# Optimization experiments

Hardware: AMD Instinct MI355X
Metric: run time of the kernel (lower is better)

## Reference

```python
import jax, jax.numpy as jnp
import numpy as np


def haar_level(x):
    """One 2D Haar (periodization-equivalent for even sizes) DWT on [B,K,C,H,W].
    Returns [B,4K,C,H/2,W/2] with per-parent band order (LL, Hx, Hy, Hxy),
    matching the tree's append order yl, yh0, yh1, yh2."""
    B, K, C, H, W = x.shape
    x = x.reshape(B, K, C, H // 2, 2, W // 2, 2)
    a = x[:, :, :, :, 0, :, 0]
    b = x[:, :, :, :, 0, :, 1]
    c = x[:, :, :, :, 1, :, 0]
    d = x[:, :, :, :, 1, :, 1]
    ll = (a + b + c + d) * 0.5
    h1 = (a - b + c - d) * 0.5   # high along width
    h2 = (a + b - c - d) * 0.5   # high along height
    h3 = (a - b - c + d) * 0.5   # diagonal
    out = jnp.stack([ll, h1, h2, h3], axis=2)  # [B,K,4,C,H/2,W/2]
    return out.reshape(B, 4 * K, C, H // 2, W // 2)


def conv2d(x, w, b, stride, pad):
    y = jax.lax.conv_general_dilated(
        x, w, window_strides=(stride, stride),
        padding=[(pad, pad), (pad, pad)],
        dimension_numbers=('NCHW', 'OIHW', 'NCHW'))
    return y + b[None, :, None, None]


def setup_inputs() -> dict:
    key = jax.random.key(0)
    ks = jax.random.split(key, 9)
    s = 0.05
    return {
        'x':        jax.random.normal(ks[0], (64, 3, 224, 224), dtype=jnp.float32),
        'w_s1':     jax.random.normal(ks[1], (192, 3, 7, 7), dtype=jnp.float32) * s,
        'b_s1':     jax.random.normal(ks[2], (192,), dtype=jnp.float32) * s,
        'w_s2':     jax.random.normal(ks[3], (192, 192, 7, 7), dtype=jnp.float32) * s,
        'b_s2':     jax.random.normal(ks[4], (192,), dtype=jnp.float32) * s,
        'w_p':      jax.random.normal(ks[5], (768, 960, 3, 3), dtype=jnp.float32) * s,
        'b_p':      jax.random.normal(ks[6], (768,), dtype=jnp.float32) * s,
        'cls_token': jax.random.normal(ks[7], (1, 1, 768), dtype=jnp.float32),
        'positions': jax.random.normal(ks[8], (50, 768), dtype=jnp.float32),
    }


def reference(x, w_s1, b_s1, w_s2, b_s2, w_p, b_p, cls_token, positions):
    B = x.shape[0]
    # ---- 4-level full Haar wavelet packet tree (vectorized over subbands) ----
    t = x[:, None]                      # [B,1,3,224,224]
    for _ in range(4):
        t = haar_level(t)               # -> [B,256,3,14,14]
    wav = t.reshape(B, 256 * 3, 14, 14)  # [B,768,14,14] (tree concat order)
    # ---- spatial branch: two strided 7x7 convs (224 -> 56 -> 14) ----
    sp = conv2d(x, w_s1, b_s1, stride=4, pad=3)
    sp = conv2d(sp, w_s2, b_s2, stride=4, pad=3)   # [B,192,14,14]
    feat = jnp.concatenate([wav, sp], axis=1)      # [B,960,14,14]
    # ---- patch projection conv 3x3 s2 -> 7x7, flatten to tokens ----
    y = conv2d(feat, w_p, b_p, stride=2, pad=1)    # [B,768,7,7]
    y = y.reshape(B, 768, 49).transpose(0, 2, 1)   # [B,49,768]
    cls = jnp.broadcast_to(cls_token, (B, 1, 768))
    y = jnp.concatenate([cls, y], axis=1) + positions  # [B,50,768]
    return y
```

## Files before the change

### kernel.cpp

```cpp
#include <hip/hip_runtime.h>
#include <stdint.h>

typedef __attribute__((ext_vector_type(8))) short short8;
typedef __attribute__((ext_vector_type(4))) float floatx4;

__device__ inline unsigned short f2bf(float f){
  union { float fv; unsigned int u; } v; v.fv = f;
  unsigned int u = v.u;
  unsigned int r = ((u >> 16) & 1u) + 0x7FFFu;
  return (unsigned short)((u + r) >> 16);
}

__device__ __forceinline__ void async16(const void* g, void* l){
  __builtin_amdgcn_global_load_lds(
      (const __attribute__((address_space(1))) unsigned int*)g,
      (__attribute__((address_space(3))) unsigned int*)l, 16, 0, 0);
}

#define PBAR(N) do {                                              \
    asm volatile("s_waitcnt vmcnt(" #N ")" ::: "memory");          \
    __builtin_amdgcn_s_barrier();                                  \
    asm volatile("" ::: "memory");                                 \
  } while (0)

__global__ void prep_w1(const float* __restrict__ w, unsigned short* __restrict__ w1p){
  int i = blockIdx.x*256 + threadIdx.x;
  if (i >= 192*192) return;
  int k = i % 192, o = i / 192;
  int cc = k >> 3, kx = k & 7;
  unsigned short v = 0;
  if (cc < 21 && kx < 7){
    int c = cc / 7, ky = cc % 7;
    v = f2bf(w[(o*3 + c)*49 + ky*7 + kx]);
  }
  w1p[i] = v;
}
__global__ void prep_w2(const float* __restrict__ w, unsigned short* __restrict__ w2p){
  int i = blockIdx.x*256 + threadIdx.x;
  if (i >= 192*9408) return;
  int k = i % 9408, o = i / 9408;
  int g = k / 192, c = k % 192;
  int ky = g / 7, kx = g % 7;
  w2p[i] = f2bf(w[((o*192 + c)*7 + ky)*7 + kx]);
}
__global__ void prep_w3(const float* __restrict__ w, unsigned short* __restrict__ w3p){
  int i = blockIdx.x*256 + threadIdx.x;
  if (i >= 768*8640) return;
  int k = i % 8640, o = i / 8640;
  int g = k / 960, c = k % 960;
  int ky = g / 3, kx = g % 3;
  w3p[i] = f2bf(w[((o*960 + c)*3 + ky)*3 + kx]);
}
__global__ void prep_zp(unsigned int* __restrict__ zp){
  zp[threadIdx.x] = 0u;
}

__global__ void pad_x2(const float* __restrict__ x, unsigned short* __restrict__ xh2){
  int idx = blockIdx.x*256 + threadIdx.x;
  if (idx >= 64*3*230*56*8) return;
  int kx = idx & 7; int t = idx >> 3;
  int ox = t % 56;  t /= 56;
  int iy = t % 230; t /= 230;
  int row = iy - 3;
  int col = 4*ox - 3 + kx;
  unsigned short v = 0;
  if (row >= 0 && row < 224 && col >= 0 && col < 224)
    v = f2bf(x[((size_t)t*224 + row)*224 + col]);
  xh2[idx] = v;
}

__global__ void wavelet_kernel(const float* __restrict__ x, unsigned short* __restrict__ feat){
  int blk = blockIdx.x;
  int j = blk % 14; blk /= 14;
  int i = blk % 14; blk /= 14;
  int c = blk % 3;  int b = blk / 3;
  int t = threadIdx.x;
  int u = t >> 4, v = t & 15;
  float val = x[((size_t)(b*3 + c)*224 + (i*16 + u))*224 + (j*16 + v)];
  #pragma unroll
  for (int bit = 1; bit < 64; bit <<= 1){
    float p = __shfl_xor(val, bit);
    val = (t & bit) ? (p - val) : (val + p);
  }
  __shared__ float s[256];
  #pragma unroll
  for (int bit = 64; bit < 256; bit <<= 1){
    s[t] = val; __syncthreads();
    float p = s[t ^ bit]; __syncthreads();
    val = (t & bit) ? (p - val) : (val + p);
  }
  s[t] = val; __syncthreads();
  int k = t;
  int d1 = (k>>6)&3, d2 = (k>>4)&3, d3 = (k>>2)&3, d4 = k&3;
  int mr = (d1>>1) | ((d2>>1)<<1) | ((d3>>1)<<2) | ((d4>>1)<<3);
  int mc = (d1&1)  | ((d2&1)<<1)  | ((d3&1)<<2)  | ((d4&1)<<3);
  float outv = s[mr*16 + mc] * 0.0625f;
  feat[((size_t)((b*14 + i)*14 + j))*960 + (k*3 + c)] = f2bf(outv);
}

__global__ __launch_bounds__(256) void conv1_gemm(const unsigned short* __restrict__ xh2,
                                                  const unsigned short* __restrict__ w1p,
                                                  const float* __restrict__ b1,
                                                  unsigned short* __restrict__ sp1){
  __shared__ unsigned short As[2][128*64], Bs[2][64*64];
  int m0 = blockIdx.x*128, n0 = blockIdx.y*64;
  int tid = threadIdx.x, wave = tid >> 6, lane = tid & 63;
  int l16 = lane & 15, quad = lane >> 4;
  int wy = wave >> 1, wx = wave & 1;
  int r8 = lane >> 3, kb = (lane & 7) ^ r8;

  int Abase[4];
  #pragma unroll
  for (int j = 0; j < 4; j++){
    int row = wave*32 + j*8 + r8;
    int m = m0 + row;
    int ox = m % 56; int t = m / 56; int oy = t % 56; int b = t / 56;
    Abase[j] = (b*690 + 4*oy)*448 + ox*8;
  }
  const unsigned short* pB0 = w1p + (n0 + wave*16 + r8)*192 + kb*8;
  const unsigned short* pB1 = pB0 + 8*192;

  int sw = l16 & 7;
  int xo0 = ((quad    ) ^ sw)*8;
  int xo1 = ((quad + 4) ^ sw)*8;
  int aoff[4];
  #pragma unroll
  for (int mt = 0; mt < 4; mt++) aoff[mt] = (wy*64 + mt*16 + l16)*64;
  int boff0 = (wx*32 + l16)*64, boff1 = boff0 + 16*64;

  floatx4 acc[4][2];
  #pragma unroll
  for (int mt = 0; mt < 4; mt++)
    #pragma unroll
    for (int nt = 0; nt < 2; nt++) acc[mt][nt] = (floatx4){0.f,0.f,0.f,0.f};

  auto stage = [&](int i, int buf){
    int cc = i*8 + kb;
    int c = (cc*147) >> 10;
    int ky = cc - 7*c;
    int koff = (c*230 + ky)*448;
    #pragma unroll
    for (int j = 0; j < 4; j++)
      async16(xh2 + Abase[j] + koff, (void*)&As[buf][(wave*32 + j*8)*64]);
    async16(pB0 + i*64, (void*)&Bs[buf][(wave*16    )*64]);
    async16(pB1 + i*64, (void*)&Bs[buf][(wave*16 + 8)*64]);
  };

  stage(0, 0);
  __syncthreads();
  #pragma unroll
  for (int i = 0; i < 3; i++){
    int buf = i & 1;
    if (i < 2) stage(i+1, buf ^ 1);
    #pragma unroll
    for (int ks = 0; ks < 2; ks++){
      int xo = ks ? xo1 : xo0;
      short8 b0 = *(const short8*)&Bs[buf][boff0 + xo];
      short8 b1 = *(const short8*)&Bs[buf][boff1 + xo];
      #pragma unroll
      for (int mt = 0; mt < 4; mt++){
        short8 a = *(const short8*)&As[buf][aoff[mt] + xo];
        acc[mt][0] = __builtin_amdgcn_mfma_f32_16x16x32_bf16(a, b0, acc[mt][0], 0, 0, 0);
        acc[mt][1] = __builtin_amdgcn_mfma_f32_16x16x32_bf16(a, b1, acc[mt][1], 0, 0, 0);
      }
    }
    __syncthreads();
  }

  #pragma unroll
  for (int mt = 0; mt < 4; mt++){
    #pragma unroll
    for (int rg = 0; rg < 4; rg++){
      int row = wy*64 + mt*16 + quad*4 + rg;
      size_t ob = (size_t)(m0 + row)*192;
      #pragma unroll
      for (int nt = 0; nt < 2; nt++){
        int nn = n0 + wx*32 + nt*16 + l16;
        sp1[ob + nn] = f2bf(acc[mt][nt][rg] + b1[nn]);
      }
    }
  }
}

template<int MODE>
__global__ __launch_bounds__(256) void conv_gemm(const unsigned short* __restrict__ Ain,
                                                 const unsigned short* __restrict__ Bt,
                                                 const float* __restrict__ bias,
                                                 const float* __restrict__ pos,
                                                 const unsigned short* __restrict__ zp,
                                                 void* __restrict__ outp){
  constexpr int OH  = (MODE==2) ? 14 : 7;
  constexpr int OW  = OH;
  constexpr int IH  = (MODE==2) ? 56 : 14;
  constexpr int IW  = IH;
  constexpr int Cin = (MODE==2) ? 192 : 960;
  constexpr int KW  = (MODE==2) ? 7 : 3;
  constexpr int S   = (MODE==2) ? 4 : 2;
  constexpr int P   = (MODE==2) ? 3 : 1;
  constexpr int K   = (MODE==2) ? 9408 : 8640;
  constexpr int NIT = K/64;
  constexpr int MTI = (MODE==2) ? 196 : 49;
  constexpr int GRP = (MODE==2) ? 24 : 96;

  int id = blockIdx.x;
  int g = id / GRP, rem = id % GRP;
  int mtile = g*8 + (rem & 7), ntile = rem >> 3;
  if (mtile >= MTI) return;
  int m0 = mtile*64, n0 = ntile*64;

  __shared__ unsigned short As[3][64*64], Bs[3][64*64];
  int tid = threadIdx.x, wave = tid >> 6, lane = tid & 63;
  int l16 = lane & 15, quad = lane >> 4;
  int wy = wave >> 1, wx = wave & 1;

  int r8 = lane >> 3, kb = (lane & 7) ^ r8;
  int rA0 = wave*16 + r8, rA1 = rA0 + 8;

  int m_0 = m0 + rA0;
  int ox0 = m_0 % OW; int t0 = m_0 / OW; int oy0 = t0 % OH; int bb0 = t0 / OH;
  int iyb0 = S*oy0 - P, ixb0 = S*ox0 - P;
  int abase0 = ((bb0*IH + iyb0)*IW + ixb0)*Cin + kb*8;
  int m_1 = m0 + rA1;
  int ox1 = m_1 % OW; int t1 = m_1 / OW; int oy1 = t1 % OH; int bb1 = t1 / OH;
  int iyb1 = S*oy1 - P, ixb1 = S*ox1 - P;
  int abase1 = ((bb1*IH + iyb1)*IW + ixb1)*Cin + kb*8;

  const unsigned short* pB0 = Bt + (size_t)(n0 + rA0)*K + kb*8;
  const unsigned short* pB1 = Bt + (size_t)(n0 + rA1)*K + kb*8;

  int sw = l16 & 7;
  int xo0 = ((quad    ) ^ sw)*8;
  int xo1 = ((quad + 4) ^ sw)*8;
  int aoff0 = (wy*32      + l16)*64;
  int aoff1 = (wy*32 + 16 + l16)*64;
  int boff0 = (wx*32      + l16)*64;
  int boff1 = (wx*32 + 16 + l16)*64;

  floatx4 acc[2][2];
  #pragma unroll
  for (int a = 0; a < 2; a++)
    #pragma unroll
    for (int bq = 0; bq < 2; bq++) acc[a][bq] = (floatx4){0.f,0.f,0.f,0.f};

  int c0 = 0, ky = 0, kx = 0, k0n = 0;

  auto stage = [&](int buf){
    int koff = (ky*IW + kx)*Cin + c0;
    int iy0 = iyb0 + ky, ix0 = ixb0 + kx;
    int iy1 = iyb1 + ky, ix1 = ixb1 + kx;
    const unsigned short* pa0 = ((unsigned)iy0 < (unsigned)IH && (unsigned)ix0 < (unsigned)IW)
                                ? (Ain + (abase0 + koff)) : zp;
    const unsigned short* pa1 = ((unsigned)iy1 < (unsigned)IH && (unsigned)ix1 < (unsigned)IW)
                                ? (Ain + (abase1 + koff)) : zp;
    async16(pa0, (void*)&As[buf][(wave*16    )*64]);
    async16(pa1, (void*)&As[buf][(wave*16 + 8)*64]);
    async16(pB0 + k0n, (void*)&Bs[buf][(wave*16    )*64]);
    async16(pB1 + k0n, (void*)&Bs[buf][(wave*16 + 8)*64]);
    k0n += 64;
    c0 += 64;
    if (c0 == Cin){ c0 = 0; kx++; if (kx == KW){ kx = 0; ky++; } }
  };

  auto compute = [&](int buf){
    #pragma unroll
    for (int ks = 0; ks < 2; ks++){
      int xo = ks ? xo1 : xo0;
      short8 a0 = *(const short8*)&As[buf][aoff0 + xo];
      short8 a1 = *(const short8*)&As[buf][aoff1 + xo];
      short8 b0 = *(const short8*)&Bs[buf][boff0 + xo];
      short8 b1 = *(const short8*)&Bs[buf][boff1 + xo];
      acc[0][0] = __builtin_amdgcn_mfma_f32_16x16x32_bf16(a0, b0, acc[0][0], 0, 0, 0);
      acc[0][1] = __builtin_amdgcn_mfma_f32_16x16x32_bf16(a0, b1, acc[0][1], 0, 0, 0);
      acc[1][0] = __builtin_amdgcn_mfma_f32_16x16x32_bf16(a1, b0, acc[1][0], 0, 0, 0);
      acc[1][1] = __builtin_amdgcn_mfma_f32_16x16x32_bf16(a1, b1, acc[1][1], 0, 0, 0);
    }
  };

  stage(0); stage(1);
  int bc = 0;
  for (int i = 0; i < NIT - 2; i++){
    PBAR(4);
    int bn = bc + 2; if (bn >= 3) bn -= 3;
    stage(bn);
    compute(bc);
    bc = (bc == 2) ? 0 : bc + 1;
  }
  PBAR(4);
  compute(bc);
  bc = (bc == 2) ? 0 : bc + 1;
  PBAR(0);
  compute(bc);

  #pragma unroll
  for (int mt = 0; mt < 2; mt++){
    #pragma unroll
    for (int rg = 0; rg < 4; rg++){
      int row = wy*32 + mt*16 + quad*4 + rg;
      int mm = m0 + row;
      #pragma unroll
      for (int nt = 0; nt < 2; nt++){
        int nn = n0 + wx*32 + nt*16 + l16;
        float v = acc[mt][nt][rg] + bias[nn];
        if (MODE == 2){
          ((unsigned short*)outp)[(size_t)mm*960 + 768 + nn] = f2bf(v);
        } else {
          int b2 = mm / 49;
          int tt = mm - b2*49;
          v += pos[(size_t)(1 + tt)*768 + nn];
          ((float*)outp)[((size_t)(mm + b2 + 1))*768 + nn] = v;
        }
      }
    }
  }
}

__global__ void cls_kernel(const float* __restrict__ cls, const float* __restrict__ pos,
                           float* __restrict__ out){
  int i = blockIdx.x*256 + threadIdx.x;
  if (i >= 64*768) return;
  int e = i % 768, b = i / 768;
  out[(size_t)(b*50)*768 + e] = cls[e] + pos[e];
}

extern "C" void kernel_launch(void* const* d_in, const int* in_sizes, int n_in,
                              void* d_out, int out_size, void* d_ws, size_t ws_size,
                              hipStream_t stream){
  (void)in_sizes; (void)n_in; (void)out_size;
  const float* x    = (const float*)d_in[0];
  const float* w_s1 = (const float*)d_in[1];
  const float* b_s1 = (const float*)d_in[2];
  const float* w_s2 = (const float*)d_in[3];
  const float* b_s2 = (const float*)d_in[4];
  const float* w_p  = (const float*)d_in[5];
  const float* b_p  = (const float*)d_in[6];
  const float* cls  = (const float*)d_in[7];
  const float* pos  = (const float*)d_in[8];
  float* out = (float*)d_out;

  char* ws = (char*)d_ws;
  if (ws_size < 118235136u) return;
  unsigned short* w1p  = (unsigned short*)(ws + 0);
  unsigned short* sp1  = (unsigned short*)(ws + 131072);
  unsigned short* zp   = (unsigned short*)(ws + 77201408u);
  unsigned short* w2p  = (unsigned short*)(ws + 77266944u);
  unsigned short* w3p  = (unsigned short*)(ws + 80879616u);
  unsigned short* feat = (unsigned short*)(ws + 94150656u);
  unsigned short* xh2  = (unsigned short*)(ws + 77266944u);

  prep_w1<<<(192*192 + 255)/256, 256, 0, stream>>>(w_s1, w1p);
  pad_x2<<<(64*3*230*56*8)/256, 256, 0, stream>>>(x, xh2);
  conv1_gemm<<<dim3(1568, 3), 256, 0, stream>>>(xh2, w1p, b_s1, sp1);
  prep_w2<<<(192*9408 + 255)/256, 256, 0, stream>>>(w_s2, w2p);
  prep_w3<<<(768*8640 + 255)/256, 256, 0, stream>>>(w_p, w3p);
  prep_zp<<<1, 64, 0, stream>>>((unsigned int*)zp);
  wavelet_kernel<<<64*3*14*14, 256, 0, stream>>>(x, feat);
  conv_gemm<2><<<600, 256, 0, stream>>>(sp1, w2p, b_s2, nullptr, zp, (void*)feat);
  conv_gemm<3><<<672, 256, 0, stream>>>(feat, w3p, b_p, pos, zp, (void*)out);
  cls_kernel<<<(64*768 + 255)/256, 256, 0, stream>>>(cls, pos, out);
}
```

Measured before the change: 425.6 us.

## Split K across waves in conv GEMM with per-wave pipelines and LDS reduction

```diff
diff --git a/kernel.cpp b/kernel.cpp
--- a/kernel.cpp
+++ b/kernel.cpp
@@ -16,12 +16,6 @@
       (const __attribute__((address_space(1))) unsigned int*)g,
       (__attribute__((address_space(3))) unsigned int*)l, 16, 0, 0);
 }
-
-#define PBAR(N) do {                                              \
-    asm volatile("s_waitcnt vmcnt(" #N ")" ::: "memory");          \
-    __builtin_amdgcn_s_barrier();                                  \
-    asm volatile("" ::: "memory");                                 \
-  } while (0)
 
 __global__ void prep_w1(const float* __restrict__ w, unsigned short* __restrict__ w1p){
   int i = blockIdx.x*256 + threadIdx.x;
@@ -198,7 +192,7 @@
   constexpr int S   = (MODE==2) ? 4 : 2;
   constexpr int P   = (MODE==2) ? 3 : 1;
   constexpr int K   = (MODE==2) ? 9408 : 8640;
-  constexpr int NIT = K/64;
+  constexpr int NSTEP = K/32;
   constexpr int MTI = (MODE==2) ? 196 : 49;
   constexpr int GRP = (MODE==2) ? 24 : 96;
 
@@ -208,108 +202,123 @@
   if (mtile >= MTI) return;
   int m0 = mtile*64, n0 = ntile*64;
 
-  __shared__ unsigned short As[3][64*64], Bs[3][64*64];
+  __shared__ unsigned short smem[32768];
+
   int tid = threadIdx.x, wave = tid >> 6, lane = tid & 63;
   int l16 = lane & 15, quad = lane >> 4;
-  int wy = wave >> 1, wx = wave & 1;
-
-  int r8 = lane >> 3, kb = (lane & 7) ^ r8;
-  int rA0 = wave*16 + r8, rA1 = rA0 + 8;
-
-  int m_0 = m0 + rA0;
-  int ox0 = m_0 % OW; int t0 = m_0 / OW; int oy0 = t0 % OH; int bb0 = t0 / OH;
-  int iyb0 = S*oy0 - P, ixb0 = S*ox0 - P;
-  int abase0 = ((bb0*IH + iyb0)*IW + ixb0)*Cin + kb*8;
-  int m_1 = m0 + rA1;
-  int ox1 = m_1 % OW; int t1 = m_1 / OW; int oy1 = t1 % OH; int bb1 = t1 / OH;
-  int iyb1 = S*oy1 - P, ixb1 = S*ox1 - P;
-  int abase1 = ((bb1*IH + iyb1)*IW + ixb1)*Cin + kb*8;
-
-  const unsigned short* pB0 = Bt + (size_t)(n0 + rA0)*K + kb*8;
-  const unsigned short* pB1 = Bt + (size_t)(n0 + rA1)*K + kb*8;
-
-  int sw = l16 & 7;
-  int xo0 = ((quad    ) ^ sw)*8;
-  int xo1 = ((quad + 4) ^ sw)*8;
-  int aoff0 = (wy*32      + l16)*64;
-  int aoff1 = (wy*32 + 16 + l16)*64;
-  int boff0 = (wx*32      + l16)*64;
-  int boff1 = (wx*32 + 16 + l16)*64;
-
-  floatx4 acc[2][2];
-  #pragma unroll
-  for (int a = 0; a < 2; a++)
-    #pragma unroll
-    for (int bq = 0; bq < 2; bq++) acc[a][bq] = (floatx4){0.f,0.f,0.f,0.f};
-
-  int c0 = 0, ky = 0, kx = 0, k0n = 0;
+
+  unsigned short* wbase = &smem[wave*8192];
+
+  int s0 = (NSTEP*wave) >> 2;
+  int s1 = (NSTEP*(wave+1)) >> 2;
+  int n = s1 - s0;
+
+  int k32 = s0*32;
+  int c0 = k32 % Cin;
+  int gk = k32 / Cin;
+  int kx = gk % KW, ky = gk / KW;
+
+  int rsub = lane >> 2;
+  int soff = ((lane & 3) ^ (rsub & 3)) * 8;
+
+  int Abase[4], iyb[4], ixb[4];
+  const unsigned short* pB[4];
+  #pragma unroll
+  for (int j = 0; j < 4; j++){
+    int R = 16*j + rsub;
+    int m = m0 + R;
+    int ox = m % OW; int t = m / OW; int oy = t % OH; int b = t / OH;
+    iyb[j] = S*oy - P; ixb[j] = S*ox - P;
+    Abase[j] = ((b*IH + iyb[j])*IW + ixb[j])*Cin;
+    pB[j] = Bt + (size_t)(n0 + R)*K + k32 + soff;
+  }
+
+  int fro = l16*32 + ((quad ^ (l16 & 3)) * 8);
+
+  floatx4 acc[4][4];
+  #pragma unroll
+  for (int mi = 0; mi < 4; mi++)
+    #pragma unroll
+    for (int ni = 0; ni < 4; ni++) acc[mi][ni] = (floatx4){0.f,0.f,0.f,0.f};
 
   auto stage = [&](int buf){
     int koff = (ky*IW + kx)*Cin + c0;
-    int iy0 = iyb0 + ky, ix0 = ixb0 + kx;
-    int iy1 = iyb1 + ky, ix1 = ixb1 + kx;
-    const unsigned short* pa0 = ((unsigned)iy0 < (unsigned)IH && (unsigned)ix0 < (unsigned)IW)
-                                ? (Ain + (abase0 + koff)) : zp;
-    const unsigned short* pa1 = ((unsigned)iy1 < (unsigned)IH && (unsigned)ix1 < (unsigned)IW)
-                                ? (Ain + (abase1 + koff)) : zp;
-    async16(pa0, (void*)&As[buf][(wave*16    )*64]);
-    async16(pa1, (void*)&As[buf][(wave*16 + 8)*64]);
-    async16(pB0 + k0n, (void*)&Bs[buf][(wave*16    )*64]);
-    async16(pB1 + k0n, (void*)&Bs[buf][(wave*16 + 8)*64]);
-    k0n += 64;
-    c0 += 64;
+    #pragma unroll
+    for (int j = 0; j < 4; j++){
+      int iy = iyb[j] + ky, ix = ixb[j] + kx;
+      bool v = ((unsigned)iy < (unsigned)IH) & ((unsigned)ix < (unsigned)IW);
+      const unsigned short* src = v ? (Ain + Abase[j] + koff + soff) : (zp + soff);
+      async16(src, (void*)(wbase + buf*2048 + j*512));
+    }
+    #pragma unroll
+    for (int j = 0; j < 4; j++){
+      async16(pB[j], (void*)(wbase + 4096 + buf*2048 + j*512));
+      pB[j] += 32;
+    }
+    c0 += 32;
     if (c0 == Cin){ c0 = 0; kx++; if (kx == KW){ kx = 0; ky++; } }
   };
 
   auto compute = [&](int buf){
-    #pragma unroll
-    for (int ks = 0; ks < 2; ks++){
-      int xo = ks ? xo1 : xo0;
-      short8 a0 = *(const short8*)&As[buf][aoff0 + xo];
-      short8 a1 = *(const short8*)&As[buf][aoff1 + xo];
-      short8 b0 = *(const short8*)&Bs[buf][boff0 + xo];
-      short8 b1 = *(const short8*)&Bs[buf][boff1 + xo];
-      acc[0][0] = __builtin_amdgcn_mfma_f32_16x16x32_bf16(a0, b0, acc[0][0], 0, 0, 0);
-      acc[0][1] = __builtin_amdgcn_mfma_f32_16x16x32_bf16(a0, b1, acc[0][1], 0, 0, 0);
-      acc[1][0] = __builtin_amdgcn_mfma_f32_16x16x32_bf16(a1, b0, acc[1][0], 0, 0, 0);
-      acc[1][1] = __builtin_amdgcn_mfma_f32_16x16x32_bf16(a1, b1, acc[1][1], 0, 0, 0);
-    }
+    const unsigned short* Ab = wbase + buf*2048;
+    const unsigned short* Bb = wbase + 4096 + buf*2048;
+    short8 a[4], b[4];
+    #pragma unroll
+    for (int i = 0; i < 4; i++){
+      a[i] = *(const short8*)&Ab[fro + i*512];
+      b[i] = *(const short8*)&Bb[fro + i*512];
+    }
+    #pragma unroll
+    for (int mi = 0; mi < 4; mi++)
+      #pragma unroll
+      for (int ni = 0; ni < 4; ni++)
+        acc[mi][ni] = __builtin_amdgcn_mfma_f32_16x16x32_bf16(a[mi], b[ni], acc[mi][ni], 0, 0, 0);
   };
 
   stage(0); stage(1);
-  int bc = 0;
-  for (int i = 0; i < NIT - 2; i++){
-    PBAR(4);
-    int bn = bc + 2; if (bn >= 3) bn -= 3;
-    stage(bn);
-    compute(bc);
-    bc = (bc == 2) ? 0 : bc + 1;
-  }
-  PBAR(4);
-  compute(bc);
-  bc = (bc == 2) ? 0 : bc + 1;
-  PBAR(0);
-  compute(bc);
-
-  #pragma unroll
-  for (int mt = 0; mt < 2; mt++){
-    #pragma unroll
-    for (int rg = 0; rg < 4; rg++){
-      int row = wy*32 + mt*16 + quad*4 + rg;
-      int mm = m0 + row;
+  for (int i = 0; i < n-2; i++){
+    asm volatile("s_waitcnt vmcnt(8)" ::: "memory");
+    compute(i & 1);
+    asm volatile("s_waitcnt lgkmcnt(0)" ::: "memory");
+    stage(i & 1);
+  }
+  asm volatile("s_waitcnt vmcnt(8)" ::: "memory");
+  compute(n & 1);
+  asm volatile("s_waitcnt vmcnt(0)" ::: "memory");
+  compute((n-1) & 1);
+
+  asm volatile("s_waitcnt lgkmcnt(0) vmcnt(0)" ::: "memory");
+  __builtin_amdgcn_sched_barrier(0);
+  float* red = (float*)wbase;
+  #pragma unroll
+  for (int mi = 0; mi < 4; mi++)
+    #pragma unroll
+    for (int ni = 0; ni < 4; ni++)
       #pragma unroll
-      for (int nt = 0; nt < 2; nt++){
-        int nn = n0 + wx*32 + nt*16 + l16;
-        float v = acc[mt][nt][rg] + bias[nn];
-        if (MODE == 2){
-          ((unsigned short*)outp)[(size_t)mm*960 + 768 + nn] = f2bf(v);
-        } else {
-          int b2 = mm / 49;
-          int tt = mm - b2*49;
-          v += pos[(size_t)(1 + tt)*768 + nn];
-          ((float*)outp)[((size_t)(mm + b2 + 1))*768 + nn] = v;
-        }
+      for (int rg = 0; rg < 4; rg++){
+        int row = mi*16 + quad*4 + rg;
+        int col = ni*16 + l16;
+        red[row*64 + col] = acc[mi][ni][rg];
       }
+  __syncthreads();
+  const float* r0 = (const float*)&smem[0];
+  const float* r1 = (const float*)&smem[8192];
+  const float* r2 = (const float*)&smem[16384];
+  const float* r3 = (const float*)&smem[24576];
+  #pragma unroll
+  for (int j = 0; j < 16; j++){
+    int e = tid + 256*j;
+    float v = r0[e] + r1[e] + r2[e] + r3[e];
+    int col = e & 63, row = e >> 6;
+    int mm = m0 + row, nn = n0 + col;
+    v += bias[nn];
+    if (MODE == 2){
+      ((unsigned short*)outp)[(size_t)mm*960 + 768 + nn] = f2bf(v);
+    } else {
+      int b2 = mm / 49;
+      int tt = mm - b2*49;
+      v += pos[(size_t)(1 + tt)*768 + nn];
+      ((float*)outp)[((size_t)(mm + b2 + 1))*768 + nn] = v;
     }
   }
 }
```

Result: slower. 484.7 us (+13.9%).

## Split K across wave pairs in conv GEMM with LDS reduction

Applied to the files above, without the earlier changes.

```diff
diff --git a/kernel.cpp b/kernel.cpp
--- a/kernel.cpp
+++ b/kernel.cpp
@@ -211,7 +211,7 @@
   __shared__ unsigned short As[3][64*64], Bs[3][64*64];
   int tid = threadIdx.x, wave = tid >> 6, lane = tid & 63;
   int l16 = lane & 15, quad = lane >> 4;
-  int wy = wave >> 1, wx = wave & 1;
+  int kh = wave >> 1, nh = wave & 1;
 
   int r8 = lane >> 3, kb = (lane & 7) ^ r8;
   int rA0 = wave*16 + r8, rA1 = rA0 + 8;
@@ -229,18 +229,18 @@
   const unsigned short* pB1 = Bt + (size_t)(n0 + rA1)*K + kb*8;
 
   int sw = l16 & 7;
-  int xo0 = ((quad    ) ^ sw)*8;
-  int xo1 = ((quad + 4) ^ sw)*8;
-  int aoff0 = (wy*32      + l16)*64;
-  int aoff1 = (wy*32 + 16 + l16)*64;
-  int boff0 = (wx*32      + l16)*64;
-  int boff1 = (wx*32 + 16 + l16)*64;
-
-  floatx4 acc[2][2];
-  #pragma unroll
-  for (int a = 0; a < 2; a++)
-    #pragma unroll
-    for (int bq = 0; bq < 2; bq++) acc[a][bq] = (floatx4){0.f,0.f,0.f,0.f};
+  int xo = ((kh*4 + quad) ^ sw)*8;
+  int aoff[4];
+  #pragma unroll
+  for (int mt = 0; mt < 4; mt++) aoff[mt] = (mt*16 + l16)*64;
+  int boff0 = (nh*32      + l16)*64;
+  int boff1 = (nh*32 + 16 + l16)*64;
+
+  floatx4 acc[4][2];
+  #pragma unroll
+  for (int mt = 0; mt < 4; mt++)
+    #pragma unroll
+    for (int nt = 0; nt < 2; nt++) acc[mt][nt] = (floatx4){0.f,0.f,0.f,0.f};
 
   int c0 = 0, ky = 0, kx = 0, k0n = 0;
 
@@ -262,18 +262,20 @@
   };
 
   auto compute = [&](int buf){
-    #pragma unroll
-    for (int ks = 0; ks < 2; ks++){
-      int xo = ks ? xo1 : xo0;
-      short8 a0 = *(const short8*)&As[buf][aoff0 + xo];
-      short8 a1 = *(const short8*)&As[buf][aoff1 + xo];
-      short8 b0 = *(const short8*)&Bs[buf][boff0 + xo];
-      short8 b1 = *(const short8*)&Bs[buf][boff1 + xo];
-      acc[0][0] = __builtin_amdgcn_mfma_f32_16x16x32_bf16(a0, b0, acc[0][0], 0, 0, 0);
-      acc[0][1] = __builtin_amdgcn_mfma_f32_16x16x32_bf16(a0, b1, acc[0][1], 0, 0, 0);
-      acc[1][0] = __builtin_amdgcn_mfma_f32_16x16x32_bf16(a1, b0, acc[1][0], 0, 0, 0);
-      acc[1][1] = __builtin_amdgcn_mfma_f32_16x16x32_bf16(a1, b1, acc[1][1], 0, 0, 0);
-    }
+    short8 b0 = *(const short8*)&Bs[buf][boff0 + xo];
+    short8 b1 = *(const short8*)&Bs[buf][boff1 + xo];
+    short8 a0 = *(const short8*)&As[buf][aoff[0] + xo];
+    short8 a1 = *(const short8*)&As[buf][aoff[1] + xo];
+    short8 a2 = *(const short8*)&As[buf][aoff[2] + xo];
+    short8 a3 = *(const short8*)&As[buf][aoff[3] + xo];
+    acc[0][0] = __builtin_amdgcn_mfma_f32_16x16x32_bf16(a0, b0, acc[0][0], 0, 0, 0);
+    acc[0][1] = __builtin_amdgcn_mfma_f32_16x16x32_bf16(a0, b1, acc[0][1], 0, 0, 0);
+    acc[1][0] = __builtin_amdgcn_mfma_f32_16x16x32_bf16(a1, b0, acc[1][0], 0, 0, 0);
+    acc[1][1] = __builtin_amdgcn_mfma_f32_16x16x32_bf16(a1, b1, acc[1][1], 0, 0, 0);
+    acc[2][0] = __builtin_amdgcn_mfma_f32_16x16x32_bf16(a2, b0, acc[2][0], 0, 0, 0);
+    acc[2][1] = __builtin_amdgcn_mfma_f32_16x16x32_bf16(a2, b1, acc[2][1], 0, 0, 0);
+    acc[3][0] = __builtin_amdgcn_mfma_f32_16x16x32_bf16(a3, b0, acc[3][0], 0, 0, 0);
+    acc[3][1] = __builtin_amdgcn_mfma_f32_16x16x32_bf16(a3, b1, acc[3][1], 0, 0, 0);
   };
 
   stage(0); stage(1);
@@ -291,23 +293,39 @@
   PBAR(0);
   compute(bc);
 
-  #pragma unroll
-  for (int mt = 0; mt < 2; mt++){
-    #pragma unroll
-    for (int rg = 0; rg < 4; rg++){
-      int row = wy*32 + mt*16 + quad*4 + rg;
-      int mm = m0 + row;
+  __syncthreads();
+  float* red = (float*)As;
+  if (kh == 1){
+    #pragma unroll
+    for (int mt = 0; mt < 4; mt++)
       #pragma unroll
-      for (int nt = 0; nt < 2; nt++){
-        int nn = n0 + wx*32 + nt*16 + l16;
-        float v = acc[mt][nt][rg] + bias[nn];
-        if (MODE == 2){
-          ((unsigned short*)outp)[(size_t)mm*960 + 768 + nn] = f2bf(v);
-        } else {
-          int b2 = mm / 49;
-          int tt = mm - b2*49;
-          v += pos[(size_t)(1 + tt)*768 + nn];
-          ((float*)outp)[((size_t)(mm + b2 + 1))*768 + nn] = v;
+      for (int nt = 0; nt < 2; nt++)
+        #pragma unroll
+        for (int rg = 0; rg < 4; rg++){
+          int row = mt*16 + quad*4 + rg;
+          red[nh*2112 + row*33 + nt*16 + l16] = acc[mt][nt][rg];
+        }
+  }
+  __syncthreads();
+  if (kh == 0){
+    #pragma unroll
+    for (int mt = 0; mt < 4; mt++){
+      #pragma unroll
+      for (int rg = 0; rg < 4; rg++){
+        int row = mt*16 + quad*4 + rg;
+        int mm = m0 + row;
+        #pragma unroll
+        for (int nt = 0; nt < 2; nt++){
+          int nn = n0 + nh*32 + nt*16 + l16;
+          float v = acc[mt][nt][rg] + red[nh*2112 + row*33 + nt*16 + l16] + bias[nn];
+          if (MODE == 2){
+            ((unsigned short*)outp)[(size_t)mm*960 + 768 + nn] = f2bf(v);
+          } else {
+            int b2 = mm / 49;
+            int tt = mm - b2*49;
+            v += pos[(size_t)(1 + tt)*768 + nn];
+            ((float*)outp)[((size_t)(mm + b2 + 1))*768 + nn] = v;
+          }
         }
       }
     }
```

Result: no change. 432.9 us (+1.7%).

## Split-K conv GEMMs with atomic fp32 partials and separate bias epilogues

Applied to the files above, without the earlier changes.

```diff
diff --git a/kernel.cpp b/kernel.cpp
--- a/kernel.cpp
+++ b/kernel.cpp
@@ -53,6 +53,10 @@
 }
 __global__ void prep_zp(unsigned int* __restrict__ zp){
   zp[threadIdx.x] = 0u;
+}
+__global__ void zero_f32(float* __restrict__ p, int n){
+  int i = blockIdx.x*256 + threadIdx.x;
+  if (i < n) p[i] = 0.f;
 }
 
 __global__ void pad_x2(const float* __restrict__ x, unsigned short* __restrict__ xh2){
@@ -183,12 +187,10 @@
 }
 
 template<int MODE>
-__global__ __launch_bounds__(256) void conv_gemm(const unsigned short* __restrict__ Ain,
-                                                 const unsigned short* __restrict__ Bt,
-                                                 const float* __restrict__ bias,
-                                                 const float* __restrict__ pos,
-                                                 const unsigned short* __restrict__ zp,
-                                                 void* __restrict__ outp){
+__global__ __launch_bounds__(256) void conv_split(const unsigned short* __restrict__ Ain,
+                                                  const unsigned short* __restrict__ Bt,
+                                                  const unsigned short* __restrict__ zp,
+                                                  float* __restrict__ pout){
   constexpr int OH  = (MODE==2) ? 14 : 7;
   constexpr int OW  = OH;
   constexpr int IH  = (MODE==2) ? 56 : 14;
@@ -198,64 +200,64 @@
   constexpr int S   = (MODE==2) ? 4 : 2;
   constexpr int P   = (MODE==2) ? 3 : 1;
   constexpr int K   = (MODE==2) ? 9408 : 8640;
-  constexpr int NIT = K/64;
-  constexpr int MTI = (MODE==2) ? 196 : 49;
-  constexpr int GRP = (MODE==2) ? 24 : 96;
+  constexpr int K3  = K/3;
+  constexpr int NB  = K3/64;
+  constexpr int MTI = (MODE==2) ? 98 : 25;
+  constexpr int NTI = (MODE==2) ? 2 : 8;
+  constexpr int M   = (MODE==2) ? 12544 : 3136;
+  constexpr int NF  = (MODE==2) ? 192 : 768;
 
   int id = blockIdx.x;
-  int g = id / GRP, rem = id % GRP;
-  int mtile = g*8 + (rem & 7), ntile = rem >> 3;
-  if (mtile >= MTI) return;
-  int m0 = mtile*64, n0 = ntile*64;
-
-  __shared__ unsigned short As[3][64*64], Bs[3][64*64];
-  int tid = threadIdx.x, wave = tid >> 6, lane = tid & 63;
+  int mtile = id % MTI;
+  int kn = id / MTI;
+  int kseg = kn / NTI, ntile = kn % NTI;
+  int m0 = mtile*128, n0 = ntile*96;
+
+  __shared__ unsigned short As[2][128*64], Bs[2][96*64];
+  int tid = threadIdx.x, wv = tid >> 6, lane = tid & 63;
   int l16 = lane & 15, quad = lane >> 4;
-  int wy = wave >> 1, wx = wave & 1;
-
+  int wy = wv >> 1, wx = wv & 1;
   int r8 = lane >> 3, kb = (lane & 7) ^ r8;
-  int rA0 = wave*16 + r8, rA1 = rA0 + 8;
-
-  int m_0 = m0 + rA0;
-  int ox0 = m_0 % OW; int t0 = m_0 / OW; int oy0 = t0 % OH; int bb0 = t0 / OH;
-  int iyb0 = S*oy0 - P, ixb0 = S*ox0 - P;
-  int abase0 = ((bb0*IH + iyb0)*IW + ixb0)*Cin + kb*8;
-  int m_1 = m0 + rA1;
-  int ox1 = m_1 % OW; int t1 = m_1 / OW; int oy1 = t1 % OH; int bb1 = t1 / OH;
-  int iyb1 = S*oy1 - P, ixb1 = S*ox1 - P;
-  int abase1 = ((bb1*IH + iyb1)*IW + ixb1)*Cin + kb*8;
-
-  const unsigned short* pB0 = Bt + (size_t)(n0 + rA0)*K + kb*8;
-  const unsigned short* pB1 = Bt + (size_t)(n0 + rA1)*K + kb*8;
-
   int sw = l16 & 7;
-  int xo0 = ((quad    ) ^ sw)*8;
-  int xo1 = ((quad + 4) ^ sw)*8;
-  int aoff0 = (wy*32      + l16)*64;
-  int aoff1 = (wy*32 + 16 + l16)*64;
-  int boff0 = (wx*32      + l16)*64;
-  int boff1 = (wx*32 + 16 + l16)*64;
-
-  floatx4 acc[2][2];
-  #pragma unroll
-  for (int a = 0; a < 2; a++)
-    #pragma unroll
-    for (int bq = 0; bq < 2; bq++) acc[a][bq] = (floatx4){0.f,0.f,0.f,0.f};
-
-  int c0 = 0, ky = 0, kx = 0, k0n = 0;
+
+  int abase[4], iyb[4], ixb[4];
+  #pragma unroll
+  for (int j = 0; j < 4; j++){
+    int r = wv*32 + j*8 + r8;
+    int m = m0 + r; if (m > M-1) m = M-1;
+    int ox = m % OW; int t = m / OW; int oy = t % OH; int bb = t / OH;
+    iyb[j] = S*oy - P; ixb[j] = S*ox - P;
+    abase[j] = ((bb*IH + iyb[j])*IW + ixb[j])*Cin + kb*8;
+  }
+  const unsigned short* pB[3];
+  #pragma unroll
+  for (int j = 0; j < 3; j++)
+    pB[j] = Bt + (size_t)(n0 + wv*24 + j*8 + r8)*K + kseg*K3 + kb*8;
+
+  int k0 = kseg*K3;
+  int c0 = k0 % Cin;
+  int gk = k0 / Cin;
+  int kx = gk % KW, ky = gk / KW;
+  int k0n = 0;
+
+  floatx4 acc[4][3];
+  #pragma unroll
+  for (int mt = 0; mt < 4; mt++)
+    #pragma unroll
+    for (int nt = 0; nt < 3; nt++) acc[mt][nt] = (floatx4){0.f,0.f,0.f,0.f};
 
   auto stage = [&](int buf){
     int koff = (ky*IW + kx)*Cin + c0;
-    int iy0 = iyb0 + ky, ix0 = ixb0 + kx;
-    int iy1 = iyb1 + ky, ix1 = ixb1 + kx;
-    const unsigned short* pa0 = ((unsigned)iy0 < (unsigned)IH && (unsigned)ix0 < (unsigned)IW)
-                                ? (Ain + (abase0 + koff)) : zp;
-    const unsigned short* pa1 = ((unsigned)iy1 < (unsigned)IH && (unsigned)ix1 < (unsigned)IW)
-                                ? (Ain + (abase1 + koff)) : zp;
-    async16(pa0, (void*)&As[buf][(wave*16    )*64]);
-    async16(pa1, (void*)&As[buf][(wave*16 + 8)*64]);
-    async16(pB0 + k0n, (void*)&Bs[buf][(wave*16    )*64]);
-    async16(pB1 + k0n, (void*)&Bs[buf][(wave*16 + 8)*64]);
+    #pragma unroll
+    for (int j = 0; j < 4; j++){
+      int iy = iyb[j] + ky, ix = ixb[j] + kx;
+      const unsigned short* pa = ((unsigned)iy < (unsigned)IH && (unsigned)ix < (unsigned)IW)
+                                 ? (Ain + abase[j] + koff) : zp;
+      async16(pa, (void*)&As[buf][(wv*32 + j*8)*64]);
+    }
+    #pragma unroll
+    for (int j = 0; j < 3; j++)
+      async16(pB[j] + k0n, (void*)&Bs[buf][(wv*24 + j*8)*64]);
     k0n += 64;
     c0 += 64;
     if (c0 == Cin){ c0 = 0; kx++; if (kx == KW){ kx = 0; ky++; } }
@@ -264,54 +266,56 @@
   auto compute = [&](int buf){
     #pragma unroll
     for (int ks = 0; ks < 2; ks++){
-      int xo = ks ? xo1 : xo0;
-      short8 a0 = *(const short8*)&As[buf][aoff0 + xo];
-      short8 a1 = *(const short8*)&As[buf][aoff1 + xo];
-      short8 b0 = *(const short8*)&Bs[buf][boff0 + xo];
-      short8 b1 = *(const short8*)&Bs[buf][boff1 + xo];
-      acc[0][0] = __builtin_amdgcn_mfma_f32_16x16x32_bf16(a0, b0, acc[0][0], 0, 0, 0);
-      acc[0][1] = __builtin_amdgcn_mfma_f32_16x16x32_bf16(a0, b1, acc[0][1], 0, 0, 0);
-      acc[1][0] = __builtin_amdgcn_mfma_f32_16x16x32_bf16(a1, b0, acc[1][0], 0, 0, 0);
-      acc[1][1] = __builtin_amdgcn_mfma_f32_16x16x32_bf16(a1, b1, acc[1][1], 0, 0, 0);
+      int xo = ((ks*4 + quad) ^ sw)*8;
+      short8 b0 = *(const short8*)&Bs[buf][(wx*48      + l16)*64 + xo];
+      short8 b1 = *(const short8*)&Bs[buf][(wx*48 + 16 + l16)*64 + xo];
+      short8 b2 = *(const short8*)&Bs[buf][(wx*48 + 32 + l16)*64 + xo];
+      #pragma unroll
+      for (int mt = 0; mt < 4; mt++){
+        short8 a = *(const short8*)&As[buf][(wy*64 + mt*16 + l16)*64 + xo];
+        acc[mt][0] = __builtin_amdgcn_mfma_f32_16x16x32_bf16(a, b0, acc[mt][0], 0, 0, 0);
+        acc[mt][1] = __builtin_amdgcn_mfma_f32_16x16x32_bf16(a, b1, acc[mt][1], 0, 0, 0);
+        acc[mt][2] = __builtin_amdgcn_mfma_f32_16x16x32_bf16(a, b2, acc[mt][2], 0, 0, 0);
+      }
     }
   };
 
-  stage(0); stage(1);
-  int bc = 0;
-  for (int i = 0; i < NIT - 2; i++){
-    PBAR(4);
-    int bn = bc + 2; if (bn >= 3) bn -= 3;
-    stage(bn);
-    compute(bc);
-    bc = (bc == 2) ? 0 : bc + 1;
-  }
-  PBAR(4);
-  compute(bc);
-  bc = (bc == 2) ? 0 : bc + 1;
+  stage(0);
   PBAR(0);
-  compute(bc);
-
-  #pragma unroll
-  for (int mt = 0; mt < 2; mt++){
+  for (int i = 0; i < NB; i++){
+    if (i + 1 < NB) stage((i+1) & 1);
+    compute(i & 1);
+    PBAR(0);
+  }
+
+  #pragma unroll
+  for (int mt = 0; mt < 4; mt++){
     #pragma unroll
     for (int rg = 0; rg < 4; rg++){
-      int row = wy*32 + mt*16 + quad*4 + rg;
+      int row = wy*64 + mt*16 + quad*4 + rg;
       int mm = m0 + row;
       #pragma unroll
-      for (int nt = 0; nt < 2; nt++){
-        int nn = n0 + wx*32 + nt*16 + l16;
-        float v = acc[mt][nt][rg] + bias[nn];
-        if (MODE == 2){
-          ((unsigned short*)outp)[(size_t)mm*960 + 768 + nn] = f2bf(v);
-        } else {
-          int b2 = mm / 49;
-          int tt = mm - b2*49;
-          v += pos[(size_t)(1 + tt)*768 + nn];
-          ((float*)outp)[((size_t)(mm + b2 + 1))*768 + nn] = v;
-        }
+      for (int nt = 0; nt < 3; nt++){
+        int nn = n0 + wx*48 + nt*16 + l16;
+        atomicAdd(&pout[(size_t)mm*NF + nn], acc[mt][nt][rg]);
       }
     }
   }
+}
+
+__global__ void comb2(const float* __restrict__ pc, const float* __restrict__ bias,
+                      unsigned short* __restrict__ feat){
+  int i = blockIdx.x*256 + threadIdx.x;
+  int n = i % 192, m = i / 192;
+  feat[(size_t)m*960 + 768 + n] = f2bf(pc[i] + bias[n]);
+}
+__global__ void comb3(const float* __restrict__ pc, const float* __restrict__ bias,
+                      const float* __restrict__ pos, float* __restrict__ out){
+  int i = blockIdx.x*256 + threadIdx.x;
+  int n = i % 768, m = i / 768;
+  int b2 = m / 49, tt = m - b2*49;
+  float v = pc[(size_t)m*768 + n] + bias[n] + pos[(size_t)(1 + tt)*768 + n];
+  out[((size_t)(m + b2 + 1))*768 + n] = v;
 }
 
 __global__ void cls_kernel(const float* __restrict__ cls, const float* __restrict__ pos,
@@ -346,15 +350,23 @@
   unsigned short* w3p  = (unsigned short*)(ws + 80879616u);
   unsigned short* feat = (unsigned short*)(ws + 94150656u);
   unsigned short* xh2  = (unsigned short*)(ws + 77266944u);
+  float* pc2 = (float*)(ws + 80879616u);
+  float* pc3 = (float*)(ws + 131072);
 
   prep_w1<<<(192*192 + 255)/256, 256, 0, stream>>>(w_s1, w1p);
   pad_x2<<<(64*3*230*56*8)/256, 256, 0, stream>>>(x, xh2);
   conv1_gemm<<<dim3(1568, 3), 256, 0, stream>>>(xh2, w1p, b_s1, sp1);
   prep_w2<<<(192*9408 + 255)/256, 256, 0, stream>>>(w_s2, w2p);
-  prep_w3<<<(768*8640 + 255)/256, 256, 0, stream>>>(w_p, w3p);
   prep_zp<<<1, 64, 0, stream>>>((unsigned int*)zp);
   wavelet_kernel<<<64*3*14*14, 256, 0, stream>>>(x, feat);
-  conv_gemm<2><<<600, 256, 0, stream>>>(sp1, w2p, b_s2, nullptr, zp, (void*)feat);
-  conv_gemm<3><<<672, 256, 0, stream>>>(feat, w3p, b_p, pos, zp, (void*)out);
+
+  zero_f32<<<9408, 256, 0, stream>>>(pc2, 12544*192);
+  conv_split<2><<<588, 256, 0, stream>>>(sp1, w2p, zp, pc2);
+  comb2<<<9408, 256, 0, stream>>>(pc2, b_s2, feat);
+
+  prep_w3<<<(768*8640 + 255)/256, 256, 0, stream>>>(w_p, w3p);
+  zero_f32<<<9600, 256, 0, stream>>>(pc3, 3200*768);
+  conv_split<3><<<600, 256, 0, stream>>>(feat, w3p, zp, pc3);
+  comb3<<<9408, 256, 0, stream>>>(pc3, b_p, pos, out);
   cls_kernel<<<(64*768 + 255)/256, 256, 0, stream>>>(cls, pos, out);
 }
```

New measurement: 486.9 us. 1.14x slower.
